# Performance work log

Measured on AMD Instinct MI355X. Metric: run time of the kernel, lower is better.

The kernel has to match this reference:

```python
import jax, jax.numpy as jnp
import numpy as np

N = 524288          # events per batch
NUM_NODES = 1_000_000
D = 64              # memory_dim


def gru_cell(x, h, W_ih, W_hh, b_ih, b_hh):
    # torch.nn.GRUCell math; gates ordered (r, z, n)
    gi = x @ W_ih.T + b_ih          # [N, 3D]
    gh = h @ W_hh.T + b_hh          # [N, 3D]
    i_r, i_z, i_n = jnp.split(gi, 3, axis=-1)
    h_r, h_z, h_n = jnp.split(gh, 3, axis=-1)
    r = jax.nn.sigmoid(i_r + h_r)
    z = jax.nn.sigmoid(i_z + h_z)
    n = jnp.tanh(i_n + r * h_n)
    return (1.0 - z) * n + z * h


def setup_inputs() -> dict:
    key = jax.random.key(0)
    ks = jax.random.split(key, 9)
    scale = 1.0 / np.sqrt(D).astype(np.float32)
    return {
        "node_ids": jax.random.randint(ks[0], (N,), 0, NUM_NODES, dtype=jnp.int64)
        if jax.config.jax_enable_x64 else jax.random.randint(ks[0], (N,), 0, NUM_NODES, dtype=jnp.int32),
        "node_embeddings": jax.random.normal(ks[1], (N, D), jnp.float32),
        "timestamps": jax.random.uniform(ks[2], (N,), jnp.float32) * 1000.0,
        "node_memory": jax.random.normal(ks[3], (NUM_NODES, D), jnp.float32) * 0.1,
        "last_update_time": jax.random.uniform(ks[4], (NUM_NODES,), jnp.float32) * 500.0,
        "W_time": jax.random.normal(ks[5], (1, D), jnp.float32) * 0.1,
        "b_time": jnp.zeros((D,), jnp.float32),
        "W_ih": jax.random.normal(ks[6], (3 * D, D), jnp.float32) * scale,
        "W_hh": jax.random.normal(ks[7], (3 * D, D), jnp.float32) * scale,
        "b_ih": jnp.zeros((3 * D,), jnp.float32),
        "b_hh": jnp.zeros((3 * D,), jnp.float32),
    }


def reference(node_ids, node_embeddings, timestamps, node_memory, last_update_time,
              W_time, b_time, W_ih, W_hh, b_ih, b_hh):
    # gather persistent state
    current_memory = node_memory[node_ids]                          # [N, D]
    time_deltas = timestamps - last_update_time[node_ids]           # [N]
    # nn.Linear(1, D): out = dt * W_time[0] + b_time
    time_encoding = time_deltas[:, None] * W_time[0] + b_time       # [N, D]
    updated_memory = gru_cell(node_embeddings + time_encoding, current_memory,
                              W_ih, W_hh, b_ih, b_hh)               # [N, D]
    # scatter write-back (detached in torch)
    new_node_memory = node_memory.at[node_ids].set(jax.lax.stop_gradient(updated_memory))
    new_last_update_time = last_update_time.at[node_ids].set(jax.lax.stop_gradient(timestamps))
    return updated_memory, new_node_memory, new_last_update_time
```

## Files before the change

### kernel.cpp

```cpp
#include <hip/hip_runtime.h>
#include <cstdint>
#include <cstddef>

#define DD 64

typedef float    f32x4  __attribute__((ext_vector_type(4)));
typedef _Float16 f16x8  __attribute__((ext_vector_type(8)));
typedef _Float16 f16x4  __attribute__((ext_vector_type(4)));

__device__ __forceinline__ float sigmoidf_(float x) {
    return 1.0f / (1.0f + __expf(-x));
}
__device__ __forceinline__ float tanh_fast(float x) {
    float ax = fabsf(x);
    float t = 1.0f - 2.0f / (1.0f + __expf(2.0f * ax));
    return copysignf(t, x);
}
__device__ __forceinline__ f32x4 MFMA(f32x4 c, f16x8 a, f16x8 b) {
    return __builtin_amdgcn_mfma_f32_16x16x32_f16(a, b, c, 0, 0, 0);
}

__global__ void k_init(int* __restrict__ winner, int num_nodes) {
    int i = blockIdx.x * blockDim.x + threadIdx.x;
    if (i < num_nodes) winner[i] = -1;
}
__global__ void k_vote(const int* __restrict__ ids, int* __restrict__ winner, int n) {
    int i = blockIdx.x * blockDim.x + threadIdx.x;
    if (i < n) atomicMax(&winner[ids[i]], i);
}

__global__ void k_prep(const float* __restrict__ Wih, const float* __restrict__ Whh,
                       _Float16* __restrict__ bhi, _Float16* __restrict__ blo)
{
    int f = blockIdx.x;
    int l = threadIdx.x;
    int g = f >> 2, s = f & 3;
    int c = g * 16 + (l & 15);
    int grp = c >> 6, d = c & 63;
    int kbase = s * 32 + (l >> 4) * 8;
    int row = (grp == 0) ? d : (grp == 1) ? 64 + d : 128 + d;

    f16x8 hv, lv;
    for (int j = 0; j < 8; ++j) {
        int k = kbase + j;
        float v;
        if (grp <= 1)      v = (k < 64) ? Wih[row * 64 + k] : Whh[row * 64 + (k - 64)];
        else if (grp == 2) v = (k < 64) ? Wih[row * 64 + k] : 0.0f;
        else               v = (k < 64) ? 0.0f : Whh[row * 64 + (k - 64)];
        _Float16 h = (_Float16)v;
        hv[j] = h;
        lv[j] = (_Float16)(v - (float)h);
    }
    size_t off = ((size_t)f * 64 + l);
    ((f16x8*)bhi)[off] = hv;
    ((f16x8*)blo)[off] = lv;
}

__global__ __launch_bounds__(256, 3) void k_gru(
    const int* __restrict__ ids,
    const float* __restrict__ emb,
    const float* __restrict__ ts,
    const float* __restrict__ mem,
    const float* __restrict__ lut,
    const float* __restrict__ Wt,
    const float* __restrict__ bt,
    const float* __restrict__ bih,
    const float* __restrict__ bhh,
    const _Float16* __restrict__ bhi,
    const _Float16* __restrict__ blo,
    const int* __restrict__ winner,
    float* __restrict__ out0,
    float* __restrict__ out1,
    int n)
{
    __shared__ _Float16 xhh[64][136];
    __shared__ _Float16 xhl[64][72];
    __shared__ int sid[64];
    __shared__ int swin[64];

    const int w    = threadIdx.x >> 6;
    const int l    = threadIdx.x & 63;
    const int col  = l & 15;
    const int rowg = l >> 4;
    const int d    = w * 16 + col;

    const float bR  = bih[d] + bhh[d];
    const float bZ  = bih[64 + d] + bhh[64 + d];
    const float bIN = bih[128 + d];
    const float bHN = bhh[128 + d];

    const f16x8* H = (const f16x8*)bhi;
    const f16x8* L = (const f16x8*)blo;
    f16x8 BRh0 = H[(size_t)(w * 4 + 0) * 64 + l];
    f16x8 BRh1 = H[(size_t)(w * 4 + 1) * 64 + l];
    f16x8 BRh2 = H[(size_t)(w * 4 + 2) * 64 + l];
    f16x8 BRh3 = H[(size_t)(w * 4 + 3) * 64 + l];
    f16x8 BRl0 = L[(size_t)(w * 4 + 0) * 64 + l];
    f16x8 BRl1 = L[(size_t)(w * 4 + 1) * 64 + l];
    f16x8 BZh0 = H[(size_t)((4 + w) * 4 + 0) * 64 + l];
    f16x8 BZh1 = H[(size_t)((4 + w) * 4 + 1) * 64 + l];
    f16x8 BZh2 = H[(size_t)((4 + w) * 4 + 2) * 64 + l];
    f16x8 BZh3 = H[(size_t)((4 + w) * 4 + 3) * 64 + l];
    f16x8 BZl0 = L[(size_t)((4 + w) * 4 + 0) * 64 + l];
    f16x8 BZl1 = L[(size_t)((4 + w) * 4 + 1) * 64 + l];
    f16x8 BIh0 = H[(size_t)((8 + w) * 4 + 0) * 64 + l];
    f16x8 BIh1 = H[(size_t)((8 + w) * 4 + 1) * 64 + l];
    f16x8 BIl0 = L[(size_t)((8 + w) * 4 + 0) * 64 + l];
    f16x8 BIl1 = L[(size_t)((8 + w) * 4 + 1) * 64 + l];
    f16x8 BHh0 = H[(size_t)((12 + w) * 4 + 2) * 64 + l];
    f16x8 BHh1 = H[(size_t)((12 + w) * 4 + 3) * 64 + l];

    const f32x4 wt4 = ((const f32x4*)Wt)[col];
    const f32x4 bt4 = ((const f32x4*)bt)[col];

    const long base = (long)blockIdx.x * 64;

    float dtA = 0.f; int idA = 0;
    if (l < 16) {
        long ev = base + w * 16 + l;
        int id = 0, win = 0; float dt = 0.f;
        if (ev < n) {
            id = ids[ev];
            dt = ts[ev] - lut[id];
            win = (winner[id] == (int)ev) ? 1 : 0;
        }
        idA = id; dtA = dt;
        sid[w * 16 + l] = id;
        swin[w * 16 + l] = win;
    }

    #pragma unroll
    for (int it = 0; it < 4; ++it) {
        int  e_loc = it * 4 + rowg;
        int  r     = w * 16 + e_loc;
        long ev    = base + r;
        int   id = __shfl(idA, e_loc);
        float dt = __shfl(dtA, e_loc);
        f32x4 xv = {0.f, 0.f, 0.f, 0.f};
        f32x4 hv = {0.f, 0.f, 0.f, 0.f};
        if (ev < n) {
            xv = __builtin_nontemporal_load(&((const f32x4*)emb)[(size_t)ev * 16 + col]);
            hv = ((const f32x4*)mem)[(size_t)id * 16 + col];
            xv.x = fmaf(dt, wt4.x, xv.x + bt4.x);
            xv.y = fmaf(dt, wt4.y, xv.y + bt4.y);
            xv.z = fmaf(dt, wt4.z, xv.z + bt4.z);
            xv.w = fmaf(dt, wt4.w, xv.w + bt4.w);
        }
        f16x4 xh, xl, hh;
        {
            _Float16 a;
            a = (_Float16)xv.x; xh[0] = a; xl[0] = (_Float16)(xv.x - (float)a);
            a = (_Float16)xv.y; xh[1] = a; xl[1] = (_Float16)(xv.y - (float)a);
            a = (_Float16)xv.z; xh[2] = a; xl[2] = (_Float16)(xv.z - (float)a);
            a = (_Float16)xv.w; xh[3] = a; xl[3] = (_Float16)(xv.w - (float)a);
            hh[0] = (_Float16)hv.x;
            hh[1] = (_Float16)hv.y;
            hh[2] = (_Float16)hv.z;
            hh[3] = (_Float16)hv.w;
        }
        *(f16x4*)&xhh[r][col * 4]      = xh;
        *(f16x4*)&xhl[r][col * 4]      = xl;
        *(f16x4*)&xhh[r][64 + col * 4] = hh;
    }
    __syncthreads();

    #pragma unroll
    for (int mt = 0; mt < 4; ++mt) {
        const int arow = mt * 16 + col;
        const int k0   = rowg * 8;
        f16x8 Ah0 = *(const f16x8*)&xhh[arow][0 * 32 + k0];
        f16x8 Ah1 = *(const f16x8*)&xhh[arow][1 * 32 + k0];
        f16x8 Ah2 = *(const f16x8*)&xhh[arow][2 * 32 + k0];
        f16x8 Ah3 = *(const f16x8*)&xhh[arow][3 * 32 + k0];
        f16x8 Al0 = *(const f16x8*)&xhl[arow][0 * 32 + k0];
        f16x8 Al1 = *(const f16x8*)&xhl[arow][1 * 32 + k0];

        f32x4 aR = {0,0,0,0}, aZ = {0,0,0,0}, aI = {0,0,0,0}, aH = {0,0,0,0};
        __builtin_amdgcn_s_setprio(1);
        aR = MFMA(aR, Ah0, BRh0); aR = MFMA(aR, Ah0, BRl0); aR = MFMA(aR, Al0, BRh0);
        aR = MFMA(aR, Ah1, BRh1); aR = MFMA(aR, Ah1, BRl1); aR = MFMA(aR, Al1, BRh1);
        aR = MFMA(aR, Ah2, BRh2); aR = MFMA(aR, Ah3, BRh3);
        aZ = MFMA(aZ, Ah0, BZh0); aZ = MFMA(aZ, Ah0, BZl0); aZ = MFMA(aZ, Al0, BZh0);
        aZ = MFMA(aZ, Ah1, BZh1); aZ = MFMA(aZ, Ah1, BZl1); aZ = MFMA(aZ, Al1, BZh1);
        aZ = MFMA(aZ, Ah2, BZh2); aZ = MFMA(aZ, Ah3, BZh3);
        aI = MFMA(aI, Ah0, BIh0); aI = MFMA(aI, Ah0, BIl0); aI = MFMA(aI, Al0, BIh0);
        aI = MFMA(aI, Ah1, BIh1); aI = MFMA(aI, Ah1, BIl1); aI = MFMA(aI, Al1, BIh1);
        aH = MFMA(aH, Ah2, BHh0); aH = MFMA(aH, Ah3, BHh1);
        __builtin_amdgcn_s_setprio(0);

        #pragma unroll
        for (int r = 0; r < 4; ++r) {
            int  eloc = mt * 16 + rowg * 4 + r;
            long ev   = base + eloc;
            if (ev < n) {
                float rr = sigmoidf_(aR[r] + bR);
                float zz = sigmoidf_(aZ[r] + bZ);
                float nn = tanh_fast(aI[r] + bIN + rr * (aH[r] + bHN));
                float hv = (float)xhh[eloc][64 + d];
                float o  = (1.f - zz) * nn + zz * hv;
                __builtin_nontemporal_store(o, &out0[(size_t)ev * 64 + d]);
                if (swin[eloc])
                    __builtin_nontemporal_store(o, &out1[(size_t)sid[eloc] * 64 + d]);
            }
        }
    }
}

__global__ void k_fill(const int* __restrict__ winner,
                       const f32x4* __restrict__ mem4,
                       f32x4* __restrict__ out14,
                       int num_nodes)
{
    int idx = blockIdx.x * blockDim.x + threadIdx.x;
    if (idx >= num_nodes * 16) return;
    int nidx = idx >> 4;
    if (winner[nidx] < 0) {
        f32x4 v = __builtin_nontemporal_load(&mem4[idx]);
        __builtin_nontemporal_store(v, &out14[idx]);
    }
}

__global__ void k_time(float* out2,
                       const float* __restrict__ ts,
                       const float* __restrict__ lut,
                       int num_nodes)
{
    int i = blockIdx.x * blockDim.x + threadIdx.x;
    if (i < num_nodes) {
        int wv = reinterpret_cast<const int*>(out2)[i];
        out2[i] = (wv >= 0) ? ts[wv] : lut[i];
    }
}

extern "C" void kernel_launch(void* const* d_in, const int* in_sizes, int n_in,
                              void* d_out, int out_size, void* d_ws, size_t ws_size,
                              hipStream_t stream) {
    const int*   ids = (const int*)  d_in[0];
    const float* emb = (const float*)d_in[1];
    const float* ts  = (const float*)d_in[2];
    const float* mem = (const float*)d_in[3];
    const float* lut = (const float*)d_in[4];
    const float* Wt  = (const float*)d_in[5];
    const float* bt  = (const float*)d_in[6];
    const float* Wih = (const float*)d_in[7];
    const float* Whh = (const float*)d_in[8];
    const float* bih = (const float*)d_in[9];
    const float* bhh = (const float*)d_in[10];

    const int N         = in_sizes[0];
    const int NUM_NODES = in_sizes[4];

    float* out0 = (float*)d_out;
    float* out1 = out0 + (size_t)N * DD;
    float* out2 = out1 + (size_t)NUM_NODES * DD;
    int*   winner = (int*)out2;

    _Float16* bfragH = (_Float16*)d_ws;
    _Float16* bfragL = bfragH + 64 * 64 * 8;

    k_init<<<(NUM_NODES + 255) / 256, 256, 0, stream>>>(winner, NUM_NODES);
    k_vote<<<(N + 255) / 256, 256, 0, stream>>>(ids, winner, N);
    k_prep<<<64, 64, 0, stream>>>(Wih, Whh, bfragH, bfragL);

    int nchunks = (N + 63) / 64;
    k_gru<<<nchunks, 256, 0, stream>>>(ids, emb, ts, mem, lut, Wt, bt, bih, bhh,
                                       bfragH, bfragL, winner, out0, out1, N);

    long vec = (long)NUM_NODES * 16;
    k_fill<<<(int)((vec + 255) / 256), 256, 0, stream>>>(
        winner, (const f32x4*)mem, (f32x4*)out1, NUM_NODES);

    k_time<<<(NUM_NODES + 255) / 256, 256, 0, stream>>>(out2, ts, lut, NUM_NODES);
}
```

Before: 244.8 us.

## Precompute per-event dt and winner flag; fuse fill and timestamp kernels

Adds a k_dt pass that computes each event's time delta and winner flag and packs them with the node id into an 8-byte record in workspace. The GRU kernel then reads that record instead of doing dependent gathers into lut and winner, and its launch bounds go from 3 to 4 blocks per CU. The separate fill and timestamp kernels are merged into one k_tail kernel, removing a launch and a second pass over the winner array. This costs an extra kernel launch and N*8 bytes of workspace traffic, and the path falls back to the old code if the workspace is too small.

```diff
diff --git a/kernel.cpp b/kernel.cpp
--- a/kernel.cpp
+++ b/kernel.cpp
@@ -5,6 +5,7 @@
 #define DD 64
 
 typedef float    f32x4  __attribute__((ext_vector_type(4)));
+typedef float    f32x2  __attribute__((ext_vector_type(2)));
 typedef _Float16 f16x8  __attribute__((ext_vector_type(8)));
 typedef _Float16 f16x4  __attribute__((ext_vector_type(4)));
 
@@ -27,6 +28,19 @@
 __global__ void k_vote(const int* __restrict__ ids, int* __restrict__ winner, int n) {
     int i = blockIdx.x * blockDim.x + threadIdx.x;
     if (i < n) atomicMax(&winner[ids[i]], i);
+}
+
+__global__ void k_dt(const int* __restrict__ ids, const float* __restrict__ ts,
+                     const float* __restrict__ lut, const int* __restrict__ winner,
+                     f32x2* __restrict__ dtw, int n) {
+    int ev = blockIdx.x * blockDim.x + threadIdx.x;
+    if (ev < n) {
+        int id = ids[ev];
+        float dt = ts[ev] - lut[id];
+        unsigned iw = (unsigned)id | ((winner[id] == ev) ? 0x80000000u : 0u);
+        f32x2 v; v.x = dt; v.y = __uint_as_float(iw);
+        dtw[ev] = v;
+    }
 }
 
 __global__ void k_prep(const float* __restrict__ Wih, const float* __restrict__ Whh,
@@ -56,7 +70,8 @@
     ((f16x8*)blo)[off] = lv;
 }
 
-__global__ __launch_bounds__(256, 3) void k_gru(
+template<bool PRE>
+__global__ __launch_bounds__(256, 4) void k_gru(
     const int* __restrict__ ids,
     const float* __restrict__ emb,
     const float* __restrict__ ts,
@@ -69,6 +84,7 @@
     const _Float16* __restrict__ bhi,
     const _Float16* __restrict__ blo,
     const int* __restrict__ winner,
+    const f32x2* __restrict__ dtw,
     float* __restrict__ out0,
     float* __restrict__ out1,
     int n)
@@ -120,9 +136,17 @@
         long ev = base + w * 16 + l;
         int id = 0, win = 0; float dt = 0.f;
         if (ev < n) {
-            id = ids[ev];
-            dt = ts[ev] - lut[id];
-            win = (winner[id] == (int)ev) ? 1 : 0;
+            if (PRE) {
+                f32x2 v = dtw[ev];
+                dt = v.x;
+                unsigned iw = __float_as_uint(v.y);
+                id  = (int)(iw & 0x7FFFFFFFu);
+                win = (int)(iw >> 31);
+            } else {
+                id = ids[ev];
+                dt = ts[ev] - lut[id];
+                win = (winner[id] == (int)ev) ? 1 : 0;
+            }
         }
         idA = id; dtA = dt;
         sid[w * 16 + l] = id;
@@ -206,30 +230,23 @@
     }
 }
 
-__global__ void k_fill(const int* __restrict__ winner,
+__global__ void k_tail(float* out2,
                        const f32x4* __restrict__ mem4,
                        f32x4* __restrict__ out14,
+                       const float* __restrict__ ts,
+                       const float* __restrict__ lut,
                        int num_nodes)
 {
     int idx = blockIdx.x * blockDim.x + threadIdx.x;
     if (idx >= num_nodes * 16) return;
     int nidx = idx >> 4;
-    if (winner[nidx] < 0) {
+    int c    = idx & 15;
+    int wv = reinterpret_cast<const int*>(out2)[nidx];
+    if (wv < 0) {
         f32x4 v = __builtin_nontemporal_load(&mem4[idx]);
         __builtin_nontemporal_store(v, &out14[idx]);
     }
-}
-
-__global__ void k_time(float* out2,
-                       const float* __restrict__ ts,
-                       const float* __restrict__ lut,
-                       int num_nodes)
-{
-    int i = blockIdx.x * blockDim.x + threadIdx.x;
-    if (i < num_nodes) {
-        int wv = reinterpret_cast<const int*>(out2)[i];
-        out2[i] = (wv >= 0) ? ts[wv] : lut[i];
-    }
+    if (c == 0) out2[nidx] = (wv >= 0) ? ts[wv] : lut[nidx];
 }
 
 extern "C" void kernel_launch(void* const* d_in, const int* in_sizes, int n_in,
@@ -257,18 +274,28 @@
 
     _Float16* bfragH = (_Float16*)d_ws;
     _Float16* bfragL = bfragH + 64 * 64 * 8;
-
+    f32x2*    dtw    = (f32x2*)((char*)d_ws + 128 * 1024);
+
+    const size_t need = 128 * 1024 + (size_t)N * 8;
+    const bool   pre  = (ws_size >= need);
+
+    k_prep<<<64, 64, 0, stream>>>(Wih, Whh, bfragH, bfragL);
     k_init<<<(NUM_NODES + 255) / 256, 256, 0, stream>>>(winner, NUM_NODES);
     k_vote<<<(N + 255) / 256, 256, 0, stream>>>(ids, winner, N);
-    k_prep<<<64, 64, 0, stream>>>(Wih, Whh, bfragH, bfragL);
 
     int nchunks = (N + 63) / 64;
-    k_gru<<<nchunks, 256, 0, stream>>>(ids, emb, ts, mem, lut, Wt, bt, bih, bhh,
-                                       bfragH, bfragL, winner, out0, out1, N);
+    if (pre) {
+        k_dt<<<(N + 255) / 256, 256, 0, stream>>>(ids, ts, lut, winner, dtw, N);
+        k_gru<true><<<nchunks, 256, 0, stream>>>(ids, emb, ts, mem, lut, Wt, bt,
+                                                 bih, bhh, bfragH, bfragL, winner,
+                                                 dtw, out0, out1, N);
+    } else {
+        k_gru<false><<<nchunks, 256, 0, stream>>>(ids, emb, ts, mem, lut, Wt, bt,
+                                                  bih, bhh, bfragH, bfragL, winner,
+                                                  dtw, out0, out1, N);
+    }
 
     long vec = (long)NUM_NODES * 16;
-    k_fill<<<(int)((vec + 255) / 256), 256, 0, stream>>>(
-        winner, (const f32x4*)mem, (f32x4*)out1, NUM_NODES);
-
-    k_time<<<(NUM_NODES + 255) / 256, 256, 0, stream>>>(out2, ts, lut, NUM_NODES);
-}
+    k_tail<<<(int)((vec + 255) / 256), 256, 0, stream>>>(
+        out2, (const f32x4*)mem, (f32x4*)out1, ts, lut, NUM_NODES);
+}
```

Measured after the change: 287.9 us. 17.6% more time.
